# Performance work log

Measured on AMD Instinct MI355X. Metric: run time of the kernel, lower is better.

The kernel has to match this reference:

```python
import jax, jax.numpy as jnp
import numpy as np

TEMPERATURE = 0.07
EPS = 1e-12  # matches F.normalize eps

def _l2norm(x, axis):
    n = jnp.sqrt(jnp.sum(x * x, axis=axis, keepdims=True))
    return x / jnp.maximum(n, EPS)

def setup_inputs() -> dict:
    key = jax.random.key(0)
    features = jax.random.normal(key, (512, 256), dtype=jnp.float32)
    return {"features": features}

def reference(features) -> jnp.ndarray:
    B = features.shape[0]
    f = _l2norm(features, axis=1)                      # [B, D]
    fi = f[:, None, :]                                 # broadcast over j
    fj = f[None, :, :]                                 # broadcast over i
    mutual = fi * fj                                   # [B, B, D]
    gate_i = fi * mutual
    gate_j = fj * mutual
    # torch broadcasting: + features adds f[j, k] along trailing dims
    feats_self_i = _l2norm(fi * gate_i + f, axis=2)
    feats_other_i = _l2norm(fi * gate_j + f, axis=2)
    feats_other_j = _l2norm(fj * gate_i + f, axis=2)
    # note: features_self_j is computed in the original but never used in any dot product

    raw_self_i = jnp.einsum('ik,ijk->ij', f, feats_self_i) / TEMPERATURE
    raw_self_j = jnp.einsum('ik,ijk->ij', f, feats_other_j) / TEMPERATURE  # (original uses other_j here)
    raw_other_i = jnp.einsum('ik,ijk->ij', f, feats_other_i) / TEMPERATURE
    raw_other_j = jnp.einsum('ik,ijk->ij', f, feats_other_j) / TEMPERATURE

    logits_mask = 1.0 - jnp.eye(B, dtype=f.dtype)      # zero out diagonal
    exp_sum = (jnp.exp(raw_self_i) + jnp.exp(raw_self_j)
               + jnp.exp(raw_other_i) + jnp.exp(raw_other_j)) * logits_mask
    vs_all = jnp.sum(exp_sum, axis=1, keepdims=True)   # [B, 1]

    log_prob = raw_self_i - jnp.log(vs_all)            # [B, B]
    mean_log_prob_pos = jnp.sum(log_prob, axis=1) / B
    loss = -jnp.mean(mean_log_prob_pos)
    return loss
```

## Files before the change

### kernel.cpp

```cpp
#include <hip/hip_runtime.h>
#include <math.h>

#define Bq 512
#define Dq 256

__device__ __forceinline__ float waveReduceSum(float v) {
    #pragma unroll
    for (int off = 32; off > 0; off >>= 1)
        v += __shfl_xor(v, off, 64);
    return v;
}

__global__ __launch_bounds__(256) void prep_kernel(
        const float* __restrict__ feat,
        float* __restrict__ fT, float* __restrict__ C1, float* __restrict__ C2,
        float* __restrict__ A1, float* __restrict__ A2) {
    int i = blockIdx.x;
    int k = threadIdx.x;
    float x = feat[i * Dq + k];
    float ss = waveReduceSum(x * x);
    __shared__ float wsum[4];
    int wid = threadIdx.x >> 6, lane = threadIdx.x & 63;
    if (lane == 0) wsum[wid] = ss;
    __syncthreads();
    float tot = wsum[0] + wsum[1] + wsum[2] + wsum[3];
    float n = fmaxf(sqrtf(tot), 1e-12f);
    float a = x / n;
    float a2 = a * a;
    float a3 = a2 * a;
    float c0 = 1.0f + a3;
    fT[k * Bq + i] = a;
    A1[i * Dq + k] = a;
    A2[i * Dq + k] = a2;
    C1[i * Dq + k] = a * c0;
    C2[i * Dq + k] = c0 * c0;
}

__global__ __launch_bounds__(256) void pair_kernel(
        const float* __restrict__ fT,
        const float* __restrict__ C1, const float* __restrict__ C2,
        const float* __restrict__ A1, const float* __restrict__ A2,
        float* __restrict__ Sv, float* __restrict__ Vv) {
    const int i = blockIdx.x;
    const int t = threadIdx.x;
    const int j0 = 2 * t;

    __shared__ __align__(16) float s_c1[Dq];
    __shared__ __align__(16) float s_c2[Dq];
    __shared__ __align__(16) float s_a1[Dq];
    __shared__ __align__(16) float s_a2[Dq];
    s_c1[t] = C1[i * Dq + t];
    s_c2[t] = C2[i * Dq + t];
    s_a1[t] = A1[i * Dq + t];
    s_a2[t] = A2[i * Dq + t];
    __syncthreads();

    const float4* __restrict__ vc1 = (const float4*)s_c1;
    const float4* __restrict__ vc2 = (const float4*)s_c2;
    const float4* __restrict__ va1 = (const float4*)s_a1;
    const float4* __restrict__ va2 = (const float4*)s_a2;

    float du0 = 0.f, nu0 = 0.f, dv0 = 0.f, nv0 = 0.f;
    float du1 = 0.f, nu1 = 0.f, dv1 = 0.f, nv1 = 0.f;

    #pragma unroll 4
    for (int k4 = 0; k4 < Dq / 4; ++k4) {
        float4 c1 = vc1[k4];
        float4 c2 = vc2[k4];
        float4 a1 = va1[k4];
        float4 a2 = va2[k4];
        const float c1a[4] = {c1.x, c1.y, c1.z, c1.w};
        const float c2a[4] = {c2.x, c2.y, c2.z, c2.w};
        const float a1a[4] = {a1.x, a1.y, a1.z, a1.w};
        const float a2a[4] = {a2.x, a2.y, a2.z, a2.w};
        #pragma unroll
        for (int kk = 0; kk < 4; ++kk) {
            int k = k4 * 4 + kk;
            float2 b2v = *(const float2*)(fT + k * Bq + j0);
            {
                float b = b2v.x;
                float bb = b * b;
                float w  = fmaf(a2a[kk], b, 1.0f);
                float wb = w * b;
                du0 = fmaf(c1a[kk], b,  du0);
                nu0 = fmaf(c2a[kk], bb, nu0);
                dv0 = fmaf(a1a[kk], wb, dv0);
                nv0 = fmaf(wb,      wb, nv0);
            }
            {
                float b = b2v.y;
                float bb = b * b;
                float w  = fmaf(a2a[kk], b, 1.0f);
                float wb = w * b;
                du1 = fmaf(c1a[kk], b,  du1);
                nu1 = fmaf(c2a[kk], bb, nu1);
                dv1 = fmaf(a1a[kk], wb, dv1);
                nv1 = fmaf(wb,      wb, nv1);
            }
        }
    }

    const float Tinv = 1.0f / 0.07f;
    float raw_s0 = du0 / fmaxf(sqrtf(nu0), 1e-12f) * Tinv;
    float raw_o0 = dv0 / fmaxf(sqrtf(nv0), 1e-12f) * Tinv;
    float raw_s1 = du1 / fmaxf(sqrtf(nu1), 1e-12f) * Tinv;
    float raw_o1 = dv1 / fmaxf(sqrtf(nv1), 1e-12f) * Tinv;

    float sS = raw_s0 + raw_s1;
    float sV = 0.f;
    if (j0 != i)     sV += expf(raw_s0) + 3.0f * expf(raw_o0);
    if (j0 + 1 != i) sV += expf(raw_s1) + 3.0f * expf(raw_o1);

    sS = waveReduceSum(sS);
    sV = waveReduceSum(sV);
    __shared__ float redS[4], redV[4];
    int wid = t >> 6, lane = t & 63;
    if (lane == 0) { redS[wid] = sS; redV[wid] = sV; }
    __syncthreads();
    if (t == 0) {
        float S = 0.f, V = 0.f;
        #pragma unroll
        for (int w2 = 0; w2 < 4; ++w2) { S += redS[w2]; V += redV[w2]; }
        Sv[i] = S;
        Vv[i] = V;
    }
}

__global__ __launch_bounds__(512) void final_kernel(
        const float* __restrict__ Sv, const float* __restrict__ Vv,
        float* __restrict__ out) {
    int i = threadIdx.x;
    float t = Sv[i] * (1.0f / Bq) - logf(Vv[i]);
    t = waveReduceSum(t);
    __shared__ float red[8];
    int wid = i >> 6, lane = i & 63;
    if (lane == 0) red[wid] = t;
    __syncthreads();
    if (i == 0) {
        float s = 0.f;
        #pragma unroll
        for (int w = 0; w < 8; ++w) s += red[w];
        out[0] = -s / (float)Bq;
    }
}

extern "C" void kernel_launch(void* const* d_in, const int* in_sizes, int n_in,
                              void* d_out, int out_size, void* d_ws, size_t ws_size,
                              hipStream_t stream) {
    const float* feat = (const float*)d_in[0];
    float* ws = (float*)d_ws;
    float* fT = ws;
    float* C1 = fT + Bq * Dq;
    float* C2 = C1 + Bq * Dq;
    float* A1 = C2 + Bq * Dq;
    float* A2 = A1 + Bq * Dq;
    float* Sv = A2 + Bq * Dq;
    float* Vv = Sv + Bq;

    prep_kernel<<<Bq, Dq, 0, stream>>>(feat, fT, C1, C2, A1, A2);
    pair_kernel<<<Bq, 256, 0, stream>>>(fT, C1, C2, A1, A2, Sv, Vv);
    final_kernel<<<1, Bq, 0, stream>>>(Sv, Vv, (float*)d_out);
}
```

Measured before the change: 77.35 us.

## Fuse final reduction into pair kernel via atomics and batch prep rows

Result: slower. 91.19 us (+17.9%).

```diff
diff --git a/kernel.cpp b/kernel.cpp
--- a/kernel.cpp
+++ b/kernel.cpp
@@ -3,6 +3,8 @@
 
 #define Bq 512
 #define Dq 256
+#define RPB 16
+#define PBLK (Bq / RPB)
 
 __device__ __forceinline__ float waveReduceSum(float v) {
     #pragma unroll
@@ -13,89 +15,111 @@
 
 __global__ __launch_bounds__(256) void prep_kernel(
         const float* __restrict__ feat,
-        float* __restrict__ fT, float* __restrict__ C1, float* __restrict__ C2,
-        float* __restrict__ A1, float* __restrict__ A2) {
-    int i = blockIdx.x;
-    int k = threadIdx.x;
-    float x = feat[i * Dq + k];
-    float ss = waveReduceSum(x * x);
-    __shared__ float wsum[4];
-    int wid = threadIdx.x >> 6, lane = threadIdx.x & 63;
-    if (lane == 0) wsum[wid] = ss;
+        float* __restrict__ fT, float* __restrict__ A1,
+        float* __restrict__ A2, float* __restrict__ C0,
+        float* __restrict__ acc, unsigned int* __restrict__ cnt) {
+    const int t = threadIdx.x;
+    const int r0 = blockIdx.x * RPB;
+    __shared__ float sm[RPB][Dq + 1];
+    __shared__ float wpart[RPB][4];
+    __shared__ float sinv[RPB];
+
+    float x[RPB];
+    #pragma unroll
+    for (int r = 0; r < RPB; ++r) x[r] = feat[(r0 + r) * Dq + t];
+
+    const int wid = t >> 6, lane = t & 63;
+    #pragma unroll
+    for (int r = 0; r < RPB; ++r) {
+        float ss = waveReduceSum(x[r] * x[r]);
+        if (lane == 0) wpart[r][wid] = ss;
+    }
     __syncthreads();
-    float tot = wsum[0] + wsum[1] + wsum[2] + wsum[3];
-    float n = fmaxf(sqrtf(tot), 1e-12f);
-    float a = x / n;
-    float a2 = a * a;
-    float a3 = a2 * a;
-    float c0 = 1.0f + a3;
-    fT[k * Bq + i] = a;
-    A1[i * Dq + k] = a;
-    A2[i * Dq + k] = a2;
-    C1[i * Dq + k] = a * c0;
-    C2[i * Dq + k] = c0 * c0;
+    if (t < RPB) {
+        float tot = wpart[t][0] + wpart[t][1] + wpart[t][2] + wpart[t][3];
+        sinv[t] = 1.0f / fmaxf(sqrtf(tot), 1e-12f);
+    }
+    __syncthreads();
+
+    #pragma unroll
+    for (int r = 0; r < RPB; ++r) {
+        float a  = x[r] * sinv[r];
+        float a2 = a * a;
+        float c0 = 1.0f + a2 * a;
+        A1[(r0 + r) * Dq + t] = a;
+        A2[(r0 + r) * Dq + t] = a2;
+        C0[(r0 + r) * Dq + t] = c0;
+        sm[r][t] = a;
+    }
+    __syncthreads();
+
+    const int rr = t & 15, kb = t >> 4;
+    #pragma unroll
+    for (int p = 0; p < 16; ++p) {
+        int k = p * 16 + kb;
+        fT[k * Bq + r0 + rr] = sm[rr][k];
+    }
+
+    if (blockIdx.x == 0 && t == 0) { *acc = 0.0f; *cnt = 0u; }
 }
 
 __global__ __launch_bounds__(256) void pair_kernel(
         const float* __restrict__ fT,
-        const float* __restrict__ C1, const float* __restrict__ C2,
         const float* __restrict__ A1, const float* __restrict__ A2,
-        float* __restrict__ Sv, float* __restrict__ Vv) {
+        const float* __restrict__ C0,
+        float* __restrict__ acc, unsigned int* __restrict__ cnt,
+        float* __restrict__ out) {
     const int i = blockIdx.x;
     const int t = threadIdx.x;
     const int j0 = 2 * t;
 
-    __shared__ __align__(16) float s_c1[Dq];
-    __shared__ __align__(16) float s_c2[Dq];
-    __shared__ __align__(16) float s_a1[Dq];
+    __shared__ __align__(16) float s_a[Dq];
     __shared__ __align__(16) float s_a2[Dq];
-    s_c1[t] = C1[i * Dq + t];
-    s_c2[t] = C2[i * Dq + t];
-    s_a1[t] = A1[i * Dq + t];
+    __shared__ __align__(16) float s_c0[Dq];
+    s_a[t]  = A1[i * Dq + t];
     s_a2[t] = A2[i * Dq + t];
+    s_c0[t] = C0[i * Dq + t];
     __syncthreads();
 
-    const float4* __restrict__ vc1 = (const float4*)s_c1;
-    const float4* __restrict__ vc2 = (const float4*)s_c2;
-    const float4* __restrict__ va1 = (const float4*)s_a1;
+    const float4* __restrict__ va  = (const float4*)s_a;
     const float4* __restrict__ va2 = (const float4*)s_a2;
+    const float4* __restrict__ vc0 = (const float4*)s_c0;
+    const float* __restrict__ pb = fT + j0;
 
     float du0 = 0.f, nu0 = 0.f, dv0 = 0.f, nv0 = 0.f;
     float du1 = 0.f, nu1 = 0.f, dv1 = 0.f, nv1 = 0.f;
 
     #pragma unroll 4
     for (int k4 = 0; k4 < Dq / 4; ++k4) {
-        float4 c1 = vc1[k4];
-        float4 c2 = vc2[k4];
-        float4 a1 = va1[k4];
-        float4 a2 = va2[k4];
-        const float c1a[4] = {c1.x, c1.y, c1.z, c1.w};
-        const float c2a[4] = {c2.x, c2.y, c2.z, c2.w};
-        const float a1a[4] = {a1.x, a1.y, a1.z, a1.w};
-        const float a2a[4] = {a2.x, a2.y, a2.z, a2.w};
+        float4 a4  = va[k4];
+        float4 q4  = va2[k4];
+        float4 c4  = vc0[k4];
+        const float aa[4] = {a4.x, a4.y, a4.z, a4.w};
+        const float qq[4] = {q4.x, q4.y, q4.z, q4.w};
+        const float cc[4] = {c4.x, c4.y, c4.z, c4.w};
         #pragma unroll
         for (int kk = 0; kk < 4; ++kk) {
             int k = k4 * 4 + kk;
-            float2 b2v = *(const float2*)(fT + k * Bq + j0);
+            float2 bv = *(const float2*)(pb + k * Bq);
             {
-                float b = b2v.x;
+                float b  = bv.x;
                 float bb = b * b;
-                float w  = fmaf(a2a[kk], b, 1.0f);
-                float wb = w * b;
-                du0 = fmaf(c1a[kk], b,  du0);
-                nu0 = fmaf(c2a[kk], bb, nu0);
-                dv0 = fmaf(a1a[kk], wb, dv0);
-                nv0 = fmaf(wb,      wb, nv0);
+                float g  = cc[kk] * b;
+                float wb = fmaf(qq[kk], bb, b);
+                du0 = fmaf(aa[kk], g,  du0);
+                nu0 = fmaf(g,      g,  nu0);
+                dv0 = fmaf(aa[kk], wb, dv0);
+                nv0 = fmaf(wb,     wb, nv0);
             }
             {
-                float b = b2v.y;
+                float b  = bv.y;
                 float bb = b * b;
-                float w  = fmaf(a2a[kk], b, 1.0f);
-                float wb = w * b;
-                du1 = fmaf(c1a[kk], b,  du1);
-                nu1 = fmaf(c2a[kk], bb, nu1);
-                dv1 = fmaf(a1a[kk], wb, dv1);
-                nv1 = fmaf(wb,      wb, nv1);
+                float g  = cc[kk] * b;
+                float wb = fmaf(qq[kk], bb, b);
+                du1 = fmaf(aa[kk], g,  du1);
+                nu1 = fmaf(g,      g,  nu1);
+                dv1 = fmaf(aa[kk], wb, dv1);
+                nv1 = fmaf(wb,     wb, nv1);
             }
         }
     }
@@ -114,33 +138,20 @@
     sS = waveReduceSum(sS);
     sV = waveReduceSum(sV);
     __shared__ float redS[4], redV[4];
-    int wid = t >> 6, lane = t & 63;
+    const int wid = t >> 6, lane = t & 63;
     if (lane == 0) { redS[wid] = sS; redV[wid] = sV; }
     __syncthreads();
     if (t == 0) {
-        float S = 0.f, V = 0.f;
-        #pragma unroll
-        for (int w2 = 0; w2 < 4; ++w2) { S += redS[w2]; V += redV[w2]; }
-        Sv[i] = S;
-        Vv[i] = V;
-    }
-}
-
-__global__ __launch_bounds__(512) void final_kernel(
-        const float* __restrict__ Sv, const float* __restrict__ Vv,
-        float* __restrict__ out) {
-    int i = threadIdx.x;
-    float t = Sv[i] * (1.0f / Bq) - logf(Vv[i]);
-    t = waveReduceSum(t);
-    __shared__ float red[8];
-    int wid = i >> 6, lane = i & 63;
-    if (lane == 0) red[wid] = t;
-    __syncthreads();
-    if (i == 0) {
-        float s = 0.f;
-        #pragma unroll
-        for (int w = 0; w < 8; ++w) s += red[w];
-        out[0] = -s / (float)Bq;
+        float S = redS[0] + redS[1] + redS[2] + redS[3];
+        float V = redV[0] + redV[1] + redV[2] + redV[3];
+        float ti = S * (1.0f / Bq) - logf(V);
+        atomicAdd(acc, ti);
+        __threadfence();
+        unsigned int old = atomicAdd(cnt, 1u);
+        if (old == Bq - 1) {
+            float tot = atomicAdd(acc, 0.0f);
+            out[0] = -tot / (float)Bq;
+        }
     }
 }
 
@@ -150,14 +161,12 @@
     const float* feat = (const float*)d_in[0];
     float* ws = (float*)d_ws;
     float* fT = ws;
-    float* C1 = fT + Bq * Dq;
-    float* C2 = C1 + Bq * Dq;
-    float* A1 = C2 + Bq * Dq;
-    float* A2 = A1 + Bq * Dq;
-    float* Sv = A2 + Bq * Dq;
-    float* Vv = Sv + Bq;
+    float* A1 = fT + (size_t)Bq * Dq;
+    float* A2 = A1 + (size_t)Bq * Dq;
+    float* C0 = A2 + (size_t)Bq * Dq;
+    float* acc = C0 + (size_t)Bq * Dq;
+    unsigned int* cnt = (unsigned int*)(acc + 1);
 
-    prep_kernel<<<Bq, Dq, 0, stream>>>(feat, fT, C1, C2, A1, A2);
-    pair_kernel<<<Bq, 256, 0, stream>>>(fT, C1, C2, A1, A2, Sv, Vv);
-    final_kernel<<<1, Bq, 0, stream>>>(Sv, Vv, (float*)d_out);
+    prep_kernel<<<PBLK, 256, 0, stream>>>(feat, fT, A1, A2, C0, acc, cnt);
+    pair_kernel<<<Bq, 256, 0, stream>>>(fT, A1, A2, C0, acc, cnt, (float*)d_out);
 }
```
